# Optimization experiments

Measured on AMD Instinct MI355X. Metric: run time of the kernel, lower is better.

The kernel has to match this reference:

```python
import jax, jax.numpy as jnp
import numpy as np

NUM_HEADS = 8
NUM_GROUPS = 32
EPS = 1e-5


def setup_inputs() -> dict:
    key = jax.random.key(0)
    ks = jax.random.split(key, 3)
    B, C, T = 4, 512, 2048
    x = jax.random.normal(ks[0], (B, C, T), dtype=jnp.float32)
    gn_gamma = jnp.ones((C,), jnp.float32)
    gn_beta = jnp.zeros((C,), jnp.float32)
    w_qkv = jax.random.normal(ks[1], (3 * C, C), jnp.float32) * (1.0 / np.sqrt(C))
    b_qkv = jnp.zeros((3 * C,), jnp.float32)
    w_proj = jax.random.normal(ks[2], (C, C), jnp.float32) * (1.0 / np.sqrt(C))
    b_proj = jnp.zeros((C,), jnp.float32)
    return {"x": x, "gn_gamma": gn_gamma, "gn_beta": gn_beta,
            "w_qkv": w_qkv, "b_qkv": b_qkv, "w_proj": w_proj, "b_proj": b_proj}


def _group_norm(x, gamma, beta):
    # x: [B, C, T]
    B, C, T = x.shape
    xg = x.reshape(B, NUM_GROUPS, (C // NUM_GROUPS) * T)
    mean = xg.mean(axis=-1, keepdims=True)
    var = xg.var(axis=-1, keepdims=True)
    xn = ((xg - mean) * jax.lax.rsqrt(var + EPS)).reshape(B, C, T)
    return xn * gamma[None, :, None] + beta[None, :, None]


def reference(x, gn_gamma, gn_beta, w_qkv, b_qkv, w_proj, b_proj):
    B, C, T = x.shape
    H = NUM_HEADS
    dh = C // H  # attn_ch
    scale = 1.0 / np.sqrt(np.sqrt(dh))

    h = _group_norm(x, gn_gamma, gn_beta)
    # 1x1 conv1d == channel matmul: [B, 3C, T]
    qkv = jnp.einsum('oc,bct->bot', w_qkv, h) + b_qkv[None, :, None]
    # tokens-major: [B, T, H, 3*dh]
    qkv = qkv.transpose(0, 2, 1).reshape(B, T, H, 3 * dh)
    q, k, v = jnp.split(qkv, 3, axis=-1)  # each [B, T, H, dh]

    weight = jnp.einsum('bthc,bshc->bhts', q * scale, k * scale)
    weight = jax.nn.softmax(weight.astype(jnp.float32), axis=-1).astype(qkv.dtype)
    out = jnp.einsum('bhts,bshc->bthc', weight, v).reshape(B, T, C)

    out = out.transpose(0, 2, 1)  # [B, C, T]
    y = jnp.einsum('oc,bct->bot', w_proj, out) + b_proj[None, :, None]
    return x + y
```

## Files before the change

kernel.cpp:

```cpp
#include <hip/hip_runtime.h>
#include <hip/hip_bf16.h>
#include <math.h>
#include <stdint.h>

#define Bb 4
#define Cc 512
#define Tt 2048
#define Hh 8

typedef __attribute__((ext_vector_type(8))) short short8;
typedef __attribute__((ext_vector_type(4))) float f32x4;
typedef __attribute__((ext_vector_type(8))) unsigned short u16x8;

__device__ __forceinline__ unsigned short f2bf(float f) {
  __hip_bfloat16 h = __float2bfloat16(f);
  unsigned short u;
  __builtin_memcpy(&u, &h, 2);
  return u;
}
__device__ __forceinline__ float bf2f(unsigned short u) {
  union { uint32_t i; float f; } v;
  v.i = (uint32_t)u << 16;
  return v.f;
}

__device__ __forceinline__ void async16(const void* g, void* l) {
  __builtin_amdgcn_global_load_lds(
      (const __attribute__((address_space(1))) uint32_t*)g,
      (__attribute__((address_space(3))) uint32_t*)l, 16, 0, 0);
}

__global__ __launch_bounds__(256) void gn_part(const float* __restrict__ x,
                                               float* __restrict__ part) {
  const int blk = blockIdx.x;
  const size_t base = (size_t)blk * 4096;
  const int tid = threadIdx.x;
  float s = 0.f, ss = 0.f;
#pragma unroll
  for (int k = 0; k < 4; ++k) {
    const float4 v = *(const float4*)(x + base + (size_t)(k * 256 + tid) * 4);
    s += v.x + v.y + v.z + v.w;
    ss += v.x * v.x + v.y * v.y + v.z * v.z + v.w * v.w;
  }
#pragma unroll
  for (int off = 32; off >= 1; off >>= 1) {
    s += __shfl_down(s, off);
    ss += __shfl_down(ss, off);
  }
  __shared__ float rs[4], rss[4];
  const int wid = tid >> 6;
  if ((tid & 63) == 0) { rs[wid] = s; rss[wid] = ss; }
  __syncthreads();
  if (tid == 0) {
    part[blk * 2] = rs[0] + rs[1] + rs[2] + rs[3];
    part[blk * 2 + 1] = rss[0] + rss[1] + rss[2] + rss[3];
  }
}

__global__ __launch_bounds__(256) void norm_trans(const float* __restrict__ x,
                                                  const float* __restrict__ part,
                                                  const float* __restrict__ gamma,
                                                  const float* __restrict__ beta,
                                                  unsigned short* __restrict__ hT) {
  __shared__ unsigned short Tl[64][72];
  const int tid = threadIdx.x;
  const int b = blockIdx.z, c0 = blockIdx.y * 64, t0 = blockIdx.x * 64;
  const int cl = tid >> 2, j16 = (tid & 3) * 16;
  const int c = c0 + cl;
  const int grp = c >> 4;
  float s = 0.f, ss = 0.f;
#pragma unroll
  for (int i = 0; i < 8; ++i) {
    s += part[(b * 256 + grp * 8 + i) * 2];
    ss += part[(b * 256 + grp * 8 + i) * 2 + 1];
  }
  const float mean = s * (1.f / 32768.f);
  const float rstd = rsqrtf(ss * (1.f / 32768.f) - mean * mean + 1e-5f);
  const float ga = gamma[c] * rstd;
  const float be = beta[c] - mean * ga;
  const float* src = x + ((size_t)b * Cc + c) * Tt + t0 + j16;
#pragma unroll
  for (int q = 0; q < 4; ++q) {
    const float4 v = *(const float4*)(src + q * 4);
    Tl[j16 + q * 4 + 0][cl] = f2bf(v.x * ga + be);
    Tl[j16 + q * 4 + 1][cl] = f2bf(v.y * ga + be);
    Tl[j16 + q * 4 + 2][cl] = f2bf(v.z * ga + be);
    Tl[j16 + q * 4 + 3][cl] = f2bf(v.w * ga + be);
  }
  __syncthreads();
  const int tl = tid >> 2, i16 = (tid & 3) * 16;
  unsigned short* dst = hT + ((size_t)b * Tt + t0 + tl) * Cc + c0 + i16;
  *(u16x8*)dst = *(const u16x8*)&Tl[tl][i16];
  *(u16x8*)(dst + 8) = *(const u16x8*)&Tl[tl][i16 + 8];
}

__global__ __launch_bounds__(256) void cvt_bf16_2(const float* __restrict__ a,
                                                  unsigned short* __restrict__ oa, int n4a,
                                                  const float* __restrict__ bsrc,
                                                  unsigned short* __restrict__ ob, int n4b) {
  const int i = blockIdx.x * 256 + threadIdx.x;
  const float* in;
  unsigned short* out;
  int idx;
  if (i < n4a) {
    in = a; out = oa; idx = i;
  } else if (i < n4a + n4b) {
    in = bsrc; out = ob; idx = i - n4a;
  } else {
    return;
  }
  const float4 v = *(const float4*)(in + (size_t)idx * 4);
  ushort4 o;
  o.x = f2bf(v.x); o.y = f2bf(v.y); o.z = f2bf(v.z); o.w = f2bf(v.w);
  *(ushort4*)(out + (size_t)idx * 4) = o;
}

template <int MODE, int BM>
__global__ __launch_bounds__(256) void gemm_mfma(const unsigned short* __restrict__ A,
                                                 const unsigned short* __restrict__ Bt,
                                                 const float* __restrict__ bias,
                                                 const float* __restrict__ res,
                                                 unsigned short* __restrict__ outb,
                                                 float* __restrict__ outf,
                                                 unsigned short* __restrict__ qkt,
                                                 int M) {
  constexpr int NA = BM / 32;
  __shared__ unsigned short SMEM[(BM + 128) * 64];
  unsigned short* Al = SMEM;
  unsigned short* Bl = SMEM + BM * 64;
  const int tid = threadIdx.x;
  const int n0 = blockIdx.x * 128, m0 = blockIdx.y * BM;
  const size_t z = blockIdx.z;
  const int l = tid & 63, il = l & 15, g = l >> 4;
  const int w = tid >> 6;
  const int wm = (w >> 1) * (BM / 2), wn = (w & 1) * 64;

  const unsigned short* Bz = Bt + z * (size_t)Tt * Cc;
  const unsigned short* Ap = A + (size_t)(m0 + (tid >> 2)) * Cc + (tid & 3) * 8;
  const unsigned short* Bp = Bz + (size_t)(n0 + (tid >> 2)) * Cc + (tid & 3) * 8;
  char* ldsA = (char*)Al + w * 1024;
  char* ldsB = (char*)Bl + w * 1024;

  f32x4 acc[NA][4] = {};
  for (int k0 = 0; k0 < Cc; k0 += 64) {
#pragma unroll
    for (int ks = 0; ks < 2; ++ks) {
      const int ko = k0 + ks * 32;
      async16(Ap + ko, ldsA + ks * (BM * 64));
      if (BM == 128) async16(Ap + (size_t)64 * Cc + ko, ldsA + ks * (BM * 64) + 4096);
      async16(Bp + ko, ldsB + ks * (128 * 64));
      async16(Bp + (size_t)64 * Cc + ko, ldsB + ks * (128 * 64) + 4096);
    }
    __syncthreads();
    __builtin_amdgcn_s_setprio(1);
#pragma unroll
    for (int ks = 0; ks < 2; ++ks) {
      short8 af[NA], bf[4];
#pragma unroll
      for (int i = 0; i < NA; ++i)
        af[i] = *(const short8*)(Al + ks * (BM * 32) + (wm + i * 16 + il) * 32 + g * 8);
#pragma unroll
      for (int j = 0; j < 4; ++j)
        bf[j] = *(const short8*)(Bl + ks * (128 * 32) + (wn + j * 16 + il) * 32 + g * 8);
#pragma unroll
      for (int i = 0; i < NA; ++i)
#pragma unroll
        for (int j = 0; j < 4; ++j)
          acc[i][j] = __builtin_amdgcn_mfma_f32_16x16x32_bf16(af[i], bf[j], acc[i][j], 0, 0, 0);
    }
    __builtin_amdgcn_s_setprio(0);
    __syncthreads();
  }

  if (MODE == 1) {
#pragma unroll
    for (int i = 0; i < NA; ++i) {
#pragma unroll
      for (int r = 0; r < 4; ++r) {
        const int m = m0 + wm + i * 16 + 4 * g + r;
        const float bv = bias[m];
#pragma unroll
        for (int j = 0; j < 4; ++j) {
          const int n = n0 + wn + j * 16 + il;
          const size_t idx = (z * (size_t)M + m) * Tt + n;
          outf[idx] = acc[i][j][r] + bv + res[idx];
        }
      }
    }
  } else {
    const int r0 = m0 + wm;
    const int sec = (r0 % 192) >> 6;
    const int hh = r0 / 192;
    if (sec == 2) {
#pragma unroll
      for (int i = 0; i < 4; ++i) {
#pragma unroll
        for (int r = 0; r < 4; ++r) {
          const int m = r0 + i * 16 + 4 * g + r;
          const float bv = bias[m];
#pragma unroll
          for (int j = 0; j < 4; ++j) {
            const int n = n0 + wn + j * 16 + il;
            outb[(z * (size_t)M + m) * Tt + n] = f2bf(acc[i][j][r] + bv);
          }
        }
      }
    } else {
      unsigned short (*Sc)[32][72] = (unsigned short(*)[32][72])SMEM;
      const float qs = (sec == 0) ? 0.125f * 1.44269504f : 1.0f;
      const size_t obase = ((size_t)(z * (Hh * 2)) + hh * 2 + sec) * Tt;
#pragma unroll
      for (int hf = 0; hf < 2; ++hf) {
#pragma unroll
        for (int i = 0; i < 4; ++i) {
          const int mloc = i * 16 + 4 * g;
          const float b0 = bias[r0 + mloc + 0];
          const float b1 = bias[r0 + mloc + 1];
          const float b2 = bias[r0 + mloc + 2];
          const float b3 = bias[r0 + mloc + 3];
#pragma unroll
          for (int j2 = 0; j2 < 2; ++j2) {
            const int j = hf * 2 + j2;
            ushort4 pkk;
            pkk.x = f2bf((acc[i][j][0] + b0) * qs);
            pkk.y = f2bf((acc[i][j][1] + b1) * qs);
            pkk.z = f2bf((acc[i][j][2] + b2) * qs);
            pkk.w = f2bf((acc[i][j][3] + b3) * qs);
            *(ushort4*)&Sc[w][j2 * 16 + il][mloc] = pkk;
          }
        }
        asm volatile("s_waitcnt lgkmcnt(0)" ::: "memory");
#pragma unroll
        for (int it = 0; it < 4; ++it) {
          const int row = it * 8 + (l >> 3);
          const int mcol = (l & 7) * 8;
          const u16x8 vv = *(const u16x8*)&Sc[w][row][mcol];
          const int tg = n0 + wn + hf * 32 + row;
          *(u16x8*)(qkt + (obase + tg) * 64 + mcol) = vv;
        }
        asm volatile("s_waitcnt lgkmcnt(0)" ::: "memory");
      }
    }
  }
}

__global__ __launch_bounds__(256, 2) void attn_mfma9(const unsigned short* __restrict__ qkt,
                                                     const unsigned short* __restrict__ qkvc,
                                                     unsigned short* __restrict__ attnoT) {
  __shared__ unsigned short KVs[2][2][64 * 64];

  const int tid = threadIdx.x;
  const int w = tid >> 6, l = tid & 63, il = l & 15, g = l >> 4;

  const int bid = blockIdx.x;
  const int swz = (bid & 7) * 64 + (bid >> 3);
  const int bh = swz >> 4, qt = swz & 15;
  const int b = bh >> 3, h = bh & 7;
  const int q0 = qt * 128;

  const unsigned short* Qb = qkt + (size_t)(bh * 2) * Tt * 64;
  const char* Kb = (const char*)(Qb + (size_t)Tt * 64);
  const char* Vb = (const char*)(qkvc + ((size_t)b * (3 * Cc) + h * 192 + 128) * Tt);

  short8 qf0[2], qf1[2];
  {
    const unsigned short* qp = Qb + (size_t)(q0 + w * 32 + il) * 64 + g * 8;
    qf0[0] = *(const short8*)qp;
    qf0[1] = *(const short8*)(qp + 32);
    qf1[0] = *(const short8*)(qp + 16 * 64);
    qf1[1] = *(const short8*)(qp + 16 * 64 + 32);
  }

  union { uint32_t u[4]; short8 v; } ones;
  ones.u[0] = ones.u[1] = ones.u[2] = ones.u[3] = 0x3F803F80u;

  float m_run0 = 0.f, m_run1 = 0.f;
  f32x4 acco0[4] = {}, acco1[4] = {};
  f32x4 acc_l0 = {}, acc_l1 = {};
  uint32_t frP0[2][4], frP1[2][4];

  const int srow = w * 16 + (l >> 3);
  const int scol = ((l & 7) ^ (l >> 3)) << 4;

  auto stage = [&](int buf, int s0) {
    char* kd = (char*)&KVs[buf][0][0] + w * 2048;
    char* vd = (char*)&KVs[buf][1][0] + w * 2048;
    async16(Kb + (size_t)(s0 + srow) * 128 + scol, kd);
    async16(Kb + (size_t)(s0 + srow + 8) * 128 + scol, kd + 1024);
    async16(Vb + (size_t)srow * (Tt * 2) + (size_t)s0 * 2 + scol, vd);
    async16(Vb + (size_t)(srow + 8) * (Tt * 2) + (size_t)s0 * 2 + scol, vd + 1024);
  };

  f32x4 accs0[4], accs1[4];
  auto qk_phase = [&](int buf) {
    const float nm0 = -m_run0, nm1 = -m_run1;
#pragma unroll
    for (int i = 0; i < 4; ++i) {
      accs0[i][0] = nm0; accs0[i][1] = nm0; accs0[i][2] = nm0; accs0[i][3] = nm0;
      accs1[i][0] = nm1; accs1[i][1] = nm1; accs1[i][2] = nm1; accs1[i][3] = nm1;
    }
    const unsigned short* Kc = &KVs[buf][0][0];
#pragma unroll
    for (int ks = 0; ks < 2; ++ks) {
#pragma unroll
      for (int i = 0; i < 4; ++i) {
        const short8 kf =
            *(const short8*)(Kc + (i * 16 + il) * 64 + ((((ks << 2) + g) ^ (il & 7)) << 3));
        accs0[i] = __builtin_amdgcn_mfma_f32_16x16x32_bf16(kf, qf0[ks], accs0[i], 0, 0, 0);
        accs1[i] = __builtin_amdgcn_mfma_f32_16x16x32_bf16(kf, qf1[ks], accs1[i], 0, 0, 0);
      }
    }
  };

  auto pv_phase = [&](int buf) {
    const unsigned short* Vc = &KVs[buf][1][0];
#pragma unroll
    for (int ks = 0; ks < 2; ++ks) {
      union { uint32_t u[4]; short8 v; } fu0, fu1;
      fu0.u[0] = frP0[ks][0]; fu0.u[1] = frP0[ks][1];
      fu0.u[2] = frP0[ks][2]; fu0.u[3] = frP0[ks][3];
      fu1.u[0] = frP1[ks][0]; fu1.u[1] = frP1[ks][1];
      fu1.u[2] = frP1[ks][2]; fu1.u[3] = frP1[ks][3];
#pragma unroll
      for (int j = 0; j < 4; ++j) {
        const short8 vf =
            *(const short8*)(Vc + (j * 16 + il) * 64 + ((((ks << 2) + g) ^ (il & 7)) << 3));
        acco0[j] = __builtin_amdgcn_mfma_f32_16x16x32_bf16(fu0.v, vf, acco0[j], 0, 0, 0);
        acco1[j] = __builtin_amdgcn_mfma_f32_16x16x32_bf16(fu1.v, vf, acco1[j], 0, 0, 0);
      }
      acc_l0 = __builtin_amdgcn_mfma_f32_16x16x32_bf16(fu0.v, ones.v, acc_l0, 0, 0, 0);
      acc_l1 = __builtin_amdgcn_mfma_f32_16x16x32_bf16(fu1.v, ones.v, acc_l1, 0, 0, 0);
    }
  };

  auto softmax_one = [&](f32x4 (&accs)[4], f32x4 (&acco)[4], f32x4& acc_l,
                         float& m_run, uint32_t (&frP)[2][4]) {
    float pmax = fmaxf(fmaxf(fmaxf(accs[0][0], accs[0][1]), accs[0][2]), accs[0][3]);
    pmax = fmaxf(pmax, fmaxf(fmaxf(accs[1][0], accs[1][1]), fmaxf(accs[1][2], accs[1][3])));
    pmax = fmaxf(pmax, fmaxf(fmaxf(accs[2][0], accs[2][1]), fmaxf(accs[2][2], accs[2][3])));
    pmax = fmaxf(pmax, fmaxf(fmaxf(accs[3][0], accs[3][1]), fmaxf(accs[3][2], accs[3][3])));

    uint32_t pk[4][2];
    if (!__all(pmax <= 8.0f)) {
      float mx = pmax;
#pragma unroll
      for (int off = 1; off < 64; off <<= 1) mx = fmaxf(mx, __shfl_xor(mx, off));
      const float alpha = __builtin_amdgcn_exp2f(-mx);
      m_run += mx;
#pragma unroll
      for (int j = 0; j < 4; ++j) acco[j] = acco[j] * alpha;
      acc_l = acc_l * alpha;
#pragma unroll
      for (int i = 0; i < 4; ++i) {
        const float p0 = __builtin_amdgcn_exp2f(accs[i][0] - mx);
        const float p1 = __builtin_amdgcn_exp2f(accs[i][1] - mx);
        const float p2 = __builtin_amdgcn_exp2f(accs[i][2] - mx);
        const float p3 = __builtin_amdgcn_exp2f(accs[i][3] - mx);
        asm("v_cvt_pk_bf16_f32 %0, %1, %2" : "=v"(pk[i][0]) : "v"(p0), "v"(p1));
        asm("v_cvt_pk_bf16_f32 %0, %1, %2" : "=v"(pk[i][1]) : "v"(p2), "v"(p3));
      }
    } else {
#pragma unroll
      for (int i = 0; i < 4; ++i) {
        const float p0 = __builtin_amdgcn_exp2f(accs[i][0]);
        const float p1 = __builtin_amdgcn_exp2f(accs[i][1]);
        const float p2 = __builtin_amdgcn_exp2f(accs[i][2]);
        const float p3 = __builtin_amdgcn_exp2f(accs[i][3]);
        asm("v_cvt_pk_bf16_f32 %0, %1, %2" : "=v"(pk[i][0]) : "v"(p0), "v"(p1));
        asm("v_cvt_pk_bf16_f32 %0, %1, %2" : "=v"(pk[i][1]) : "v"(p2), "v"(p3));
      }
    }
#pragma unroll
    for (int ks = 0; ks < 2; ++ks) {
#pragma unroll
      for (int hh = 0; hh < 2; ++hh) {
        uint32_t a = pk[2 * ks][hh], bq = pk[2 * ks + 1][hh];
        asm("v_permlane32_swap_b32 %0, %1" : "+v"(a), "+v"(bq));
        asm("v_permlane16_swap_b32 %0, %1" : "+v"(a), "+v"(bq));
        frP[ks][hh] = a;
        frP[ks][2 + hh] = bq;
      }
    }
  };

  stage(0, 0);
  __syncthreads();
  stage(1, 64);
  __builtin_amdgcn_s_setprio(1);
  qk_phase(0);
  __builtin_amdgcn_s_setprio(0);
  softmax_one(accs0, acco0, acc_l0, m_run0, frP0);
  softmax_one(accs1, acco1, acc_l1, m_run1, frP1);

  const int NT = Tt / 64;
  for (int t = 1; t < NT; ++t) {
    const int cb = t & 1, pb = cb ^ 1;
    __syncthreads();
    __builtin_amdgcn_s_setprio(1);
    qk_phase(cb);
    pv_phase(pb);
    __builtin_amdgcn_s_setprio(0);
    __syncthreads();
    if (t + 1 < NT) stage(pb, (t + 1) * 64);
    softmax_one(accs0, acco0, acc_l0, m_run0, frP0);
    softmax_one(accs1, acco1, acc_l1, m_run1, frP1);
  }
  __builtin_amdgcn_s_setprio(1);
  pv_phase(1);
  __builtin_amdgcn_s_setprio(0);

#pragma unroll
  for (int r = 0; r < 4; ++r) {
    const float li0 = 1.f / acc_l0[r];
    const float li1 = 1.f / acc_l1[r];
    const int tq = q0 + w * 32 + 4 * g + r;
    unsigned short* d0 = attnoT + ((size_t)b * Tt + tq) * Cc + h * 64 + il;
    unsigned short* d1 = attnoT + ((size_t)b * Tt + tq + 16) * Cc + h * 64 + il;
#pragma unroll
    for (int j = 0; j < 4; ++j) {
      d0[j * 16] = f2bf(acco0[j][r] * li0);
      d1[j * 16] = f2bf(acco1[j][r] * li1);
    }
  }
}

extern "C" void kernel_launch(void* const* d_in, const int* in_sizes, int n_in,
                              void* d_out, int out_size, void* d_ws, size_t ws_size,
                              hipStream_t stream) {
  const float* x = (const float*)d_in[0];
  const float* gamma = (const float*)d_in[1];
  const float* beta = (const float*)d_in[2];
  const float* w_qkv = (const float*)d_in[3];
  const float* b_qkv = (const float*)d_in[4];
  const float* w_proj = (const float*)d_in[5];
  const float* b_proj = (const float*)d_in[6];
  float* out = (float*)d_out;

  char* p = (char*)d_ws;
  float* part = (float*)p;                   p += 2048 * sizeof(float);
  unsigned short* hT = (unsigned short*)p;   p += (size_t)Bb * Tt * Cc * 2;
  unsigned short* wq = (unsigned short*)p;   p += (size_t)3 * Cc * Cc * 2;
  unsigned short* wp = (unsigned short*)p;   p += (size_t)Cc * Cc * 2;
  unsigned short* qkvc = (unsigned short*)p; p += (size_t)Bb * 3 * Cc * Tt * 2;
  unsigned short* qkt = (unsigned short*)p;  p += (size_t)Bb * Hh * 2 * Tt * 64 * 2;
  unsigned short* attnoT = (unsigned short*)p;

  const int n4q = 3 * Cc * Cc / 4, n4p = Cc * Cc / 4;

  gn_part<<<dim3(1024), 256, 0, stream>>>(x, part);
  norm_trans<<<dim3(Tt / 64, Cc / 64, Bb), 256, 0, stream>>>(x, part, gamma, beta, hT);
  cvt_bf16_2<<<dim3((n4q + n4p + 255) / 256), 256, 0, stream>>>(w_qkv, wq, n4q, w_proj, wp, n4p);
  gemm_mfma<0, 128><<<dim3(Tt / 128, (3 * Cc) / 128, Bb), 256, 0, stream>>>(
      wq, hT, b_qkv, nullptr, qkvc, nullptr, qkt, 3 * Cc);
  attn_mfma9<<<dim3(512), 256, 0, stream>>>(qkt, qkvc, attnoT);
  gemm_mfma<1, 64><<<dim3(Tt / 128, Cc / 64, Bb), 256, 0, stream>>>(
      wp, attnoT, b_proj, x, nullptr, out, nullptr, Cc);
}
```

Baseline: 99.80 us.

## Software-pipeline first-half softmax across iterations to overlap with QK MFMAs

The attention loop now keeps two sets of score accumulators (A/B ping-pong) and unrolls the loop by two. The softmax for the first 16-row query half of the previous tile runs between the current tile's QK MFMAs and the PV MFMAs. This lets exp and permlane work interleave with matrix-core work instead of running after it. The first half switches to an explicit running-max scheme (scores accumulated from zero, then rescaled relative to m_run0), while the second half keeps the original pre-subtracted scheme. The extra accumulator registers raise VGPR pressure under the 2-blocks-per-SM launch bound and could cause spills.

```diff
diff --git a/kernel.cpp b/kernel.cpp
--- a/kernel.cpp
+++ b/kernel.cpp
@@ -244,9 +244,9 @@
   }
 }
 
-__global__ __launch_bounds__(256, 2) void attn_mfma9(const unsigned short* __restrict__ qkt,
-                                                     const unsigned short* __restrict__ qkvc,
-                                                     unsigned short* __restrict__ attnoT) {
+__global__ __launch_bounds__(256, 2) void attn_mfma10(const unsigned short* __restrict__ qkt,
+                                                      const unsigned short* __restrict__ qkvc,
+                                                      unsigned short* __restrict__ attnoT) {
   __shared__ unsigned short KVs[2][2][64 * 64];
 
   const int tid = threadIdx.x;
@@ -278,6 +278,8 @@
   f32x4 acco0[4] = {}, acco1[4] = {};
   f32x4 acc_l0 = {}, acc_l1 = {};
   uint32_t frP0[2][4], frP1[2][4];
+
+  f32x4 accsA0[4], accsA1[4], accsB0[4], accsB1[4];
 
   const int srow = w * 16 + (l >> 3);
   const int scol = ((l & 7) ^ (l >> 3)) << 4;
@@ -291,13 +293,12 @@
     async16(Vb + (size_t)(srow + 8) * (Tt * 2) + (size_t)s0 * 2 + scol, vd + 1024);
   };
 
-  f32x4 accs0[4], accs1[4];
-  auto qk_phase = [&](int buf) {
-    const float nm0 = -m_run0, nm1 = -m_run1;
+  auto qk_phase = [&](int buf, f32x4 (&a0)[4], f32x4 (&a1)[4]) {
+    const float nm1 = -m_run1;
 #pragma unroll
     for (int i = 0; i < 4; ++i) {
-      accs0[i][0] = nm0; accs0[i][1] = nm0; accs0[i][2] = nm0; accs0[i][3] = nm0;
-      accs1[i][0] = nm1; accs1[i][1] = nm1; accs1[i][2] = nm1; accs1[i][3] = nm1;
+      a0[i][0] = 0.f; a0[i][1] = 0.f; a0[i][2] = 0.f; a0[i][3] = 0.f;
+      a1[i][0] = nm1; a1[i][1] = nm1; a1[i][2] = nm1; a1[i][3] = nm1;
     }
     const unsigned short* Kc = &KVs[buf][0][0];
 #pragma unroll
@@ -306,14 +307,13 @@
       for (int i = 0; i < 4; ++i) {
         const short8 kf =
             *(const short8*)(Kc + (i * 16 + il) * 64 + ((((ks << 2) + g) ^ (il & 7)) << 3));
-        accs0[i] = __builtin_amdgcn_mfma_f32_16x16x32_bf16(kf, qf0[ks], accs0[i], 0, 0, 0);
-        accs1[i] = __builtin_amdgcn_mfma_f32_16x16x32_bf16(kf, qf1[ks], accs1[i], 0, 0, 0);
+        a0[i] = __builtin_amdgcn_mfma_f32_16x16x32_bf16(kf, qf0[ks], a0[i], 0, 0, 0);
+        a1[i] = __builtin_amdgcn_mfma_f32_16x16x32_bf16(kf, qf1[ks], a1[i], 0, 0, 0);
       }
     }
   };
 
   auto pv_phase = [&](int buf) {
-    const unsigned short* Vc = &KVs[buf][1][0];
 #pragma unroll
     for (int ks = 0; ks < 2; ++ks) {
       union { uint32_t u[4]; short8 v; } fu0, fu1;
@@ -324,7 +324,7 @@
 #pragma unroll
       for (int j = 0; j < 4; ++j) {
         const short8 vf =
-            *(const short8*)(Vc + (j * 16 + il) * 64 + ((((ks << 2) + g) ^ (il & 7)) << 3));
+            *(const short8*)(&KVs[buf][1][0] + (j * 16 + il) * 64 + ((((ks << 2) + g) ^ (il & 7)) << 3));
         acco0[j] = __builtin_amdgcn_mfma_f32_16x16x32_bf16(fu0.v, vf, acco0[j], 0, 0, 0);
         acco1[j] = __builtin_amdgcn_mfma_f32_16x16x32_bf16(fu1.v, vf, acco1[j], 0, 0, 0);
       }
@@ -333,23 +333,63 @@
     }
   };
 
-  auto softmax_one = [&](f32x4 (&accs)[4], f32x4 (&acco)[4], f32x4& acc_l,
-                         float& m_run, uint32_t (&frP)[2][4]) {
+  auto softmax0 = [&](f32x4 (&accs)[4]) {
     float pmax = fmaxf(fmaxf(fmaxf(accs[0][0], accs[0][1]), accs[0][2]), accs[0][3]);
     pmax = fmaxf(pmax, fmaxf(fmaxf(accs[1][0], accs[1][1]), fmaxf(accs[1][2], accs[1][3])));
     pmax = fmaxf(pmax, fmaxf(fmaxf(accs[2][0], accs[2][1]), fmaxf(accs[2][2], accs[2][3])));
     pmax = fmaxf(pmax, fmaxf(fmaxf(accs[3][0], accs[3][1]), fmaxf(accs[3][2], accs[3][3])));
 
+    if (!__all(pmax <= m_run0 + 8.0f)) {
+      float mx = pmax;
+#pragma unroll
+      for (int off = 1; off < 64; off <<= 1) mx = fmaxf(mx, __shfl_xor(mx, off));
+      const float mnew = fmaxf(m_run0, mx);
+      const float alpha = __builtin_amdgcn_exp2f(m_run0 - mnew);
+      m_run0 = mnew;
+#pragma unroll
+      for (int j = 0; j < 4; ++j) acco0[j] = acco0[j] * alpha;
+      acc_l0 = acc_l0 * alpha;
+    }
+    const float m0 = m_run0;
+    uint32_t pk[4][2];
+#pragma unroll
+    for (int i = 0; i < 4; ++i) {
+      const float p0 = __builtin_amdgcn_exp2f(accs[i][0] - m0);
+      const float p1 = __builtin_amdgcn_exp2f(accs[i][1] - m0);
+      const float p2 = __builtin_amdgcn_exp2f(accs[i][2] - m0);
+      const float p3 = __builtin_amdgcn_exp2f(accs[i][3] - m0);
+      asm("v_cvt_pk_bf16_f32 %0, %1, %2" : "=v"(pk[i][0]) : "v"(p0), "v"(p1));
+      asm("v_cvt_pk_bf16_f32 %0, %1, %2" : "=v"(pk[i][1]) : "v"(p2), "v"(p3));
+    }
+#pragma unroll
+    for (int ks = 0; ks < 2; ++ks) {
+#pragma unroll
+      for (int hh = 0; hh < 2; ++hh) {
+        uint32_t a = pk[2 * ks][hh], bq = pk[2 * ks + 1][hh];
+        asm("v_permlane32_swap_b32 %0, %1" : "+v"(a), "+v"(bq));
+        asm("v_permlane16_swap_b32 %0, %1" : "+v"(a), "+v"(bq));
+        frP0[ks][hh] = a;
+        frP0[ks][2 + hh] = bq;
+      }
+    }
+  };
+
+  auto softmax1 = [&](f32x4 (&accs)[4]) {
+    float pmax = fmaxf(fmaxf(fmaxf(accs[0][0], accs[0][1]), accs[0][2]), accs[0][3]);
+    pmax = fmaxf(pmax, fmaxf(fmaxf(accs[1][0], accs[1][1]), fmaxf(accs[1][2], accs[1][3])));
+    pmax = fmaxf(pmax, fmaxf(fmaxf(accs[2][0], accs[2][1]), fmaxf(accs[2][2], accs[2][3])));
+    pmax = fmaxf(pmax, fmaxf(fmaxf(accs[3][0], accs[3][1]), fmaxf(accs[3][2], accs[3][3])));
+
     uint32_t pk[4][2];
     if (!__all(pmax <= 8.0f)) {
       float mx = pmax;
 #pragma unroll
       for (int off = 1; off < 64; off <<= 1) mx = fmaxf(mx, __shfl_xor(mx, off));
       const float alpha = __builtin_amdgcn_exp2f(-mx);
-      m_run += mx;
-#pragma unroll
-      for (int j = 0; j < 4; ++j) acco[j] = acco[j] * alpha;
-      acc_l = acc_l * alpha;
+      m_run1 += mx;
+#pragma unroll
+      for (int j = 0; j < 4; ++j) acco1[j] = acco1[j] * alpha;
+      acc_l1 = acc_l1 * alpha;
 #pragma unroll
       for (int i = 0; i < 4; ++i) {
         const float p0 = __builtin_amdgcn_exp2f(accs[i][0] - mx);
@@ -377,34 +417,40 @@
         uint32_t a = pk[2 * ks][hh], bq = pk[2 * ks + 1][hh];
         asm("v_permlane32_swap_b32 %0, %1" : "+v"(a), "+v"(bq));
         asm("v_permlane16_swap_b32 %0, %1" : "+v"(a), "+v"(bq));
-        frP[ks][hh] = a;
-        frP[ks][2 + hh] = bq;
-      }
-    }
+        frP1[ks][hh] = a;
+        frP1[ks][2 + hh] = bq;
+      }
+    }
+  };
+
+  const int NT = Tt / 64;
+
+  auto body = [&](int t, f32x4 (&cur0)[4], f32x4 (&cur1)[4], f32x4 (&prv0)[4]) {
+    const int cb = t & 1, pb = cb ^ 1;
+    __syncthreads();
+    __builtin_amdgcn_s_setprio(1);
+    qk_phase(cb, cur0, cur1);
+    softmax0(prv0);
+    pv_phase(pb);
+    __builtin_amdgcn_s_setprio(0);
+    __syncthreads();
+    if (t + 1 < NT) stage(pb, (t + 1) * 64);
+    softmax1(cur1);
   };
 
   stage(0, 0);
   __syncthreads();
   stage(1, 64);
   __builtin_amdgcn_s_setprio(1);
-  qk_phase(0);
+  qk_phase(0, accsA0, accsA1);
   __builtin_amdgcn_s_setprio(0);
-  softmax_one(accs0, acco0, acc_l0, m_run0, frP0);
-  softmax_one(accs1, acco1, acc_l1, m_run1, frP1);
-
-  const int NT = Tt / 64;
-  for (int t = 1; t < NT; ++t) {
-    const int cb = t & 1, pb = cb ^ 1;
-    __syncthreads();
-    __builtin_amdgcn_s_setprio(1);
-    qk_phase(cb);
-    pv_phase(pb);
-    __builtin_amdgcn_s_setprio(0);
-    __syncthreads();
-    if (t + 1 < NT) stage(pb, (t + 1) * 64);
-    softmax_one(accs0, acco0, acc_l0, m_run0, frP0);
-    softmax_one(accs1, acco1, acc_l1, m_run1, frP1);
-  }
+  softmax1(accsA1);
+
+  for (int tt = 1; tt < NT; tt += 2) {
+    body(tt, accsB0, accsB1, accsA0);
+    if (tt + 1 < NT) body(tt + 1, accsA0, accsA1, accsB0);
+  }
+  softmax0(accsB0);
   __builtin_amdgcn_s_setprio(1);
   pv_phase(1);
   __builtin_amdgcn_s_setprio(0);
@@ -452,7 +498,7 @@
   cvt_bf16_2<<<dim3((n4q + n4p + 255) / 256), 256, 0, stream>>>(w_qkv, wq, n4q, w_proj, wp, n4p);
   gemm_mfma<0, 128><<<dim3(Tt / 128, (3 * Cc) / 128, Bb), 256, 0, stream>>>(
       wq, hT, b_qkv, nullptr, qkvc, nullptr, qkt, 3 * Cc);
-  attn_mfma9<<<dim3(512), 256, 0, stream>>>(qkt, qkvc, attnoT);
+  attn_mfma10<<<dim3(512), 256, 0, stream>>>(qkt, qkvc, attnoT);
   gemm_mfma<1, 64><<<dim3(Tt / 128, Cc / 64, Bb), 256, 0, stream>>>(
       wp, attnoT, b_proj, x, nullptr, out, nullptr, Cc);
 }
```

Measured after the change: 96.68 us. 1.03x faster.
